# Kernel optimization log

Hardware: AMD Instinct MI355X
Metric: run time of the kernel (lower is better)

## Reference

```python
import jax, jax.numpy as jnp
import numpy as np


def _next_pow2(n: int) -> int:
    return 1 << (int(n) - 1).bit_length()


def setup_inputs() -> dict:
    key = jax.random.key(0)
    k1, k2 = jax.random.split(key)
    B, T, L = 256, 65536, 65536  # batch, seq_len, filter length (L >= T so epoched recurrence == full causal conv)
    x = jax.random.normal(k1, (B, T), dtype=jnp.float32)
    filt = jax.random.normal(k2, (1, L), dtype=jnp.float32) / np.float32(np.sqrt(L))
    return {"x": x, "filt": filt}


def reference(x, filt):
    """EpochedFutureFill.forward == causal FIR convolution of x with filt.

    The torch module's per-token loop (sliced dot-product + FFT-refreshed
    FutureFill cache every K steps) computes exactly
        y[:, t] = sum_{s=0}^{t} filt[0, s] * x[:, t - s]
    for t < T <= L. We express that directly as one FFT convolution,
    mirroring the module's own future_fill (pow-2 rfft/irfft) math.
    """
    B, T = x.shape
    L = filt.shape[-1]
    n_fft = _next_pow2(T + L - 1)
    xf = jnp.fft.rfft(x, n=n_fft)        # (B, n_fft//2+1) complex
    ff = jnp.fft.rfft(filt, n=n_fft)     # (1, n_fft//2+1) complex, broadcasts over batch
    y_full = jnp.fft.irfft(xf * ff, n=n_fft)
    return y_full[:, :T]                 # causal part: (B, T)
```

## Files before the change

### kernel.cpp

```cpp
#include <hip/hip_runtime.h>


#define N_FFT 131072
#define N1    512
#define N2    256
#define T_LEN 65536
#define CB    128
#define PI_F  3.14159265358979323846f
#define R2_F  0.70710678118654752f
#define C16F  0.92387953251128675613f
#define S16F  0.38268343236508977173f

typedef __attribute__((ext_vector_type(2))) __fp16 h2;
typedef __attribute__((ext_vector_type(4))) __fp16 h4;
typedef __attribute__((ext_vector_type(8))) __fp16 h8;

__device__ inline int brev9(int x) { return (int)(__brev((unsigned)x) >> 23); }

__device__ inline float2 cadd(float2 a, float2 b){ return make_float2(a.x+b.x, a.y+b.y); }
__device__ inline float2 csub(float2 a, float2 b){ return make_float2(a.x-b.x, a.y-b.y); }
__device__ inline float2 cmul(float2 a, float2 b){ return make_float2(a.x*b.x-a.y*b.y, a.x*b.y+a.y*b.x); }
__device__ inline float2 cmulc(float2 a, float2 b){ return make_float2(a.x*b.x+a.y*b.y, a.y*b.x-a.x*b.y); }
__device__ inline float2 csq(float2 a){ return make_float2(a.x*a.x-a.y*a.y, 2.f*a.x*a.y); }
__device__ inline float2 conjf(float2 a){ return make_float2(a.x, -a.y); }
__device__ inline float2 expif(float a){ float s,c; __sincosf(a,&s,&c); return make_float2(c,s); }
__device__ inline h2 f2h(float2 v){ return __builtin_amdgcn_cvt_pkrtz(v.x, v.y); }

__device__ inline float2 mul_mi(float2 a){ return make_float2(a.y, -a.x); }
__device__ inline float2 mul_pi(float2 a){ return make_float2(-a.y, a.x); }
__device__ inline float2 mul_w81(float2 a){ return make_float2(R2_F*(a.x+a.y), R2_F*(a.y-a.x)); }
__device__ inline float2 mul_w83(float2 a){ return make_float2(R2_F*(a.y-a.x), -R2_F*(a.x+a.y)); }
__device__ inline float2 mul_w81c(float2 a){ return make_float2(R2_F*(a.x-a.y), R2_F*(a.x+a.y)); }
__device__ inline float2 mul_w83c(float2 a){ return make_float2(-R2_F*(a.x+a.y), R2_F*(a.x-a.y)); }

__device__ inline void dif4(float2&a0, float2&a1, float2&a2, float2&a3, float2 w1, float2 w2){
    float2 s02 = cadd(a0,a2), d02 = csub(a0,a2);
    float2 s13 = cadd(a1,a3), d13 = csub(a1,a3);
    float2 b2 = cmul(w1,d02);
    float2 t  = cmul(w1,d13);
    float2 b3 = make_float2(t.y, -t.x);
    a0 = cadd(s02,s13);
    a1 = cmul(w2, csub(s02,s13));
    a2 = cadd(b2,b3);
    a3 = cmul(w2, csub(b2,b3));
}

__device__ inline void dit4i(float2&a0, float2&a1, float2&a2, float2&a3, float2 w1, float2 w2){
    float2 t1 = cmul(w1,a1), t3 = cmul(w1,a3);
    float2 u0 = cadd(a0,t1), u1 = csub(a0,t1);
    float2 u2 = cadd(a2,t3), u3 = csub(a2,t3);
    float2 s2 = cmul(w2,u2), s3 = cmul(w2,u3);
    a0 = cadd(u0,s2); a2 = csub(u0,s2);
    a1 = make_float2(u1.x - s3.y, u1.y + s3.x);
    a3 = make_float2(u1.x + s3.y, u1.y - s3.x);
}

__device__ constexpr int BR[16] = {0,8,4,12,2,10,6,14,1,9,5,13,3,11,7,15};

__device__ __forceinline__ void fft16_fwd(float2 v[16]){
    {
        float2 s02=cadd(v[0],v[8]),  d02=csub(v[0],v[8]);
        float2 s13=cadd(v[4],v[12]), d13=csub(v[4],v[12]);
        float2 b3 = mul_mi(d13);
        v[0]=cadd(s02,s13); v[4]=csub(s02,s13);
        v[8]=cadd(d02,b3);  v[12]=csub(d02,b3);
    }
    {
        float2 s02=cadd(v[1],v[9]),  d02=csub(v[1],v[9]);
        float2 s13=cadd(v[5],v[13]), d13=csub(v[5],v[13]);
        const float2 w1 = make_float2(C16F,-S16F);
        float2 b2 = cmul(w1,d02), b3 = mul_mi(cmul(w1,d13));
        v[1]=cadd(s02,s13);  v[5]=mul_w81(csub(s02,s13));
        v[9]=cadd(b2,b3);    v[13]=mul_w81(csub(b2,b3));
    }
    {
        float2 s02=cadd(v[2],v[10]), d02=csub(v[2],v[10]);
        float2 s13=cadd(v[6],v[14]), d13=csub(v[6],v[14]);
        float2 b2 = mul_w81(d02), b3 = mul_mi(mul_w81(d13));
        v[2]=cadd(s02,s13);  v[6]=mul_mi(csub(s02,s13));
        v[10]=cadd(b2,b3);   v[14]=mul_mi(csub(b2,b3));
    }
    {
        float2 s02=cadd(v[3],v[11]), d02=csub(v[3],v[11]);
        float2 s13=cadd(v[7],v[15]), d13=csub(v[7],v[15]);
        const float2 w1 = make_float2(S16F,-C16F);
        float2 b2 = cmul(w1,d02), b3 = mul_mi(cmul(w1,d13));
        v[3]=cadd(s02,s13);  v[7]=mul_w83(csub(s02,s13));
        v[11]=cadd(b2,b3);   v[15]=mul_w83(csub(b2,b3));
    }
#pragma unroll
    for (int q=0;q<4;q++){
        float2 a0=v[4*q],a1=v[4*q+1],a2=v[4*q+2],a3=v[4*q+3];
        float2 s02=cadd(a0,a2), d02=csub(a0,a2);
        float2 s13=cadd(a1,a3), d13=csub(a1,a3);
        float2 b3 = mul_mi(d13);
        v[4*q]=cadd(s02,s13);   v[4*q+1]=csub(s02,s13);
        v[4*q+2]=cadd(d02,b3);  v[4*q+3]=csub(d02,b3);
    }
}

__device__ __forceinline__ void fft16_fwd_z8(float2 v[16]){
    {
        float2 a=v[0], b=v[4];
        float2 ib = mul_mi(b);
        v[0]=cadd(a,b); v[4]=csub(a,b);
        v[8]=cadd(a,ib); v[12]=csub(a,ib);
    }
    {
        float2 a=v[1], b=v[5];
        const float2 w1 = make_float2(C16F,-S16F);
        float2 wa = cmul(w1,a), wb = mul_mi(cmul(w1,b));
        v[1]=cadd(a,b);   v[5]=mul_w81(csub(a,b));
        v[9]=cadd(wa,wb); v[13]=mul_w81(csub(wa,wb));
    }
    {
        float2 a=v[2], b=v[6];
        float2 wa = mul_w81(a), wb = mul_mi(mul_w81(b));
        v[2]=cadd(a,b);    v[6]=mul_mi(csub(a,b));
        v[10]=cadd(wa,wb); v[14]=mul_mi(csub(wa,wb));
    }
    {
        float2 a=v[3], b=v[7];
        const float2 w1 = make_float2(S16F,-C16F);
        float2 wa = cmul(w1,a), wb = mul_mi(cmul(w1,b));
        v[3]=cadd(a,b);    v[7]=mul_w83(csub(a,b));
        v[11]=cadd(wa,wb); v[15]=mul_w83(csub(wa,wb));
    }
#pragma unroll
    for (int q=0;q<4;q++){
        float2 a0=v[4*q],a1=v[4*q+1],a2=v[4*q+2],a3=v[4*q+3];
        float2 s02=cadd(a0,a2), d02=csub(a0,a2);
        float2 s13=cadd(a1,a3), d13=csub(a1,a3);
        float2 b3 = mul_mi(d13);
        v[4*q]=cadd(s02,s13);   v[4*q+1]=csub(s02,s13);
        v[4*q+2]=cadd(d02,b3);  v[4*q+3]=csub(d02,b3);
    }
}

__device__ __forceinline__ void fft16_inv(float2 v[16]){
#pragma unroll
    for (int q=0;q<4;q++){
        float2 a0=v[4*q],a1=v[4*q+1],a2=v[4*q+2],a3=v[4*q+3];
        float2 u0=cadd(a0,a1), u1=csub(a0,a1);
        float2 u2=cadd(a2,a3), u3=csub(a2,a3);
        v[4*q]=cadd(u0,u2);   v[4*q+2]=csub(u0,u2);
        v[4*q+1]=make_float2(u1.x-u3.y, u1.y+u3.x);
        v[4*q+3]=make_float2(u1.x+u3.y, u1.y-u3.x);
    }
    {
        float2 t1=v[4], t3=v[12];
        float2 u0=cadd(v[0],t1), u1=csub(v[0],t1);
        float2 u2=cadd(v[8],t3), u3=csub(v[8],t3);
        v[0]=cadd(u0,u2); v[8]=csub(u0,u2);
        v[4]=make_float2(u1.x-u3.y, u1.y+u3.x);
        v[12]=make_float2(u1.x+u3.y, u1.y-u3.x);
    }
    {
        float2 t1=mul_w81c(v[5]), t3=mul_w81c(v[13]);
        float2 u0=cadd(v[1],t1), u1=csub(v[1],t1);
        float2 u2=cadd(v[9],t3), u3=csub(v[9],t3);
        const float2 w2 = make_float2(C16F,S16F);
        float2 s2=cmul(w2,u2), s3=cmul(w2,u3);
        v[1]=cadd(u0,s2); v[9]=csub(u0,s2);
        v[5]=make_float2(u1.x-s3.y, u1.y+s3.x);
        v[13]=make_float2(u1.x+s3.y, u1.y-s3.x);
    }
    {
        float2 t1=mul_pi(v[6]), t3=mul_pi(v[14]);
        float2 u0=cadd(v[2],t1), u1=csub(v[2],t1);
        float2 u2=cadd(v[10],t3), u3=csub(v[10],t3);
        float2 s2=mul_w81c(u2), s3=mul_w81c(u3);
        v[2]=cadd(u0,s2); v[10]=csub(u0,s2);
        v[6]=make_float2(u1.x-s3.y, u1.y+s3.x);
        v[14]=make_float2(u1.x+s3.y, u1.y-s3.x);
    }
    {
        float2 t1=mul_w83c(v[7]), t3=mul_w83c(v[15]);
        float2 u0=cadd(v[3],t1), u1=csub(v[3],t1);
        float2 u2=cadd(v[11],t3), u3=csub(v[11],t3);
        const float2 w2 = make_float2(S16F,C16F);
        float2 s2=cmul(w2,u2), s3=cmul(w2,u3);
        v[3]=cadd(u0,s2); v[11]=csub(u0,s2);
        v[7]=make_float2(u1.x-s3.y, u1.y+s3.x);
        v[15]=make_float2(u1.x+s3.y, u1.y-s3.x);
    }
}

#define XPC 34
#define XPN 546

template<bool HALF>
__global__ __launch_bounds__(256, 4) void fwd_cols(
    const float* __restrict__ re_base, const float* __restrict__ im_base,
    long long row_stride, void* __restrict__ dstv)
{
    __shared__ __align__(16) float2 s[8 * XPN + 32 * 17];
    const int tid = threadIdx.x;
    const int tile = blockIdx.x, row = blockIdx.y;
    const int n2base = tile * 8;
    float2* tab = s + 8 * XPN;

    {
        int q = tid >> 4, c = tid & 15;
        tab[q * 17 + c]        = expif((float)(q * c) * (-2.f * PI_F / 512.f));
        tab[(q + 16) * 17 + c] = expif((float)((q + 16) * c) * (-2.f * PI_F / 512.f));
    }
    __syncthreads();

    const int n2l = tid & 7, q = tid >> 3;
    const float* rp = re_base + (long long)row * row_stride;
    const float* ip = im_base ? (im_base + (long long)row * row_stride) : nullptr;

    float2 v[16];
    if (ip) {
#pragma unroll
        for (int p = 0; p < 8; p++) {
            int g = (32 * p + q) * N2 + n2base + n2l;
            v[p] = make_float2(rp[g], ip[g]);
        }
    } else {
#pragma unroll
        for (int p = 0; p < 8; p++) {
            int g = (32 * p + q) * N2 + n2base + n2l;
            v[p] = make_float2(rp[g], 0.f);
        }
    }
    fft16_fwd_z8(v);

#pragma unroll
    for (int c = 1; c < 16; c++) v[BR[c]] = cmul(v[BR[c]], tab[q * 17 + c]);
#pragma unroll
    for (int c = 0; c < 16; c++) s[n2l * XPN + c * XPC + q] = v[BR[c]];
    __syncthreads();

    const int sI = tid >> 3;
    const int cc = sI & 15, jj = sI >> 4;
    const float4* z4 = (const float4*)(s + n2l * XPN + cc * XPC);
    float2 b[16];
    if (jj == 0) {
#pragma unroll
        for (int k = 0; k < 8; k++) {
            float4 A = z4[k], B = z4[k + 8];
            b[2*k]   = make_float2(A.x + B.x, A.y + B.y);
            b[2*k+1] = make_float2(A.z + B.z, A.w + B.w);
        }
    } else {
        constexpr float CT[16] = {
            1.f, 0.98078528040323044913f, 0.92387953251128675613f, 0.83146961230254523708f,
            0.70710678118654752440f, 0.55557023301960222474f, 0.38268343236508977173f,
            0.19509032201612826785f, 0.f, -0.19509032201612826785f, -0.38268343236508977173f,
            -0.55557023301960222474f, -0.70710678118654752440f, -0.83146961230254523708f,
            -0.92387953251128675613f, -0.98078528040323044913f };
        constexpr float ST[16] = {
            0.f, -0.19509032201612826785f, -0.38268343236508977173f, -0.55557023301960222474f,
            -0.70710678118654752440f, -0.83146961230254523708f, -0.92387953251128675613f,
            -0.98078528040323044913f, -1.f, -0.98078528040323044913f, -0.92387953251128675613f,
            -0.83146961230254523708f, -0.70710678118654752440f, -0.55557023301960222474f,
            -0.38268343236508977173f, -0.19509032201612826785f };
#pragma unroll
        for (int k = 0; k < 8; k++) {
            float4 A = z4[k], B = z4[k + 8];
            float2 d0 = make_float2(A.x - B.x, A.y - B.y);
            float2 d1 = make_float2(A.z - B.z, A.w - B.w);
            b[2*k]   = (k == 0) ? d0 : cmul(d0, make_float2(CT[2*k], ST[2*k]));
            b[2*k+1] = cmul(d1, make_float2(CT[2*k+1], ST[2*k+1]));
        }
    }
    fft16_fwd(b);

    const int n2 = n2base + n2l;
    const float th = -2.f * PI_F / (float)N_FFT;
    float2 w   = expif(th * (float)(n2 * (cc + 16 * jj)));
    float2 stp = expif(th * (float)(32 * n2));
#pragma unroll
    for (int m = 0; m < 16; m++) {
        float2 rv = cmul(b[BR[m]], w);
        int k1 = cc + 32 * m + 16 * jj;
        if (HALF) {
            h2* drow = (h2*)dstv + (size_t)row * N_FFT;
            drow[(size_t)k1 * N2 + n2] = f2h(rv);
        } else {
            float2* drow = (float2*)dstv + (size_t)row * N_FFT;
            drow[(size_t)k1 * N2 + n2] = rv;
        }
        if (m < 15) w = cmul(w, stp);
    }
}

#define RPITCH 18

__global__ __launch_bounds__(128) void fwd_rows_g(float2* __restrict__ G)
{
    __shared__ __align__(16) float2 s[8 * 16 * RPITCH + 16 * RPITCH];
    const int tid = threadIdx.x;
    const int t = tid & 15, rl = tid >> 4;
    const long long row = (long long)blockIdx.x * 8 + rl;
    float2* tab = s + 8 * 16 * RPITCH;

    {
        int b0 = tid >> 4, c0 = tid & 15;
        tab[b0 * RPITCH + c0] = expif((float)(b0 * c0) * (-2.f * PI_F / 256.f));
        int e = tid + 128, b1 = e >> 4, c1 = e & 15;
        tab[b1 * RPITCH + c1] = expif((float)(b1 * c1) * (-2.f * PI_F / 256.f));
    }
    __syncthreads();

    const float2* gp = G + (size_t)row * N2 + t;
    float2 v[16];
#pragma unroll
    for (int a = 0; a < 16; a++) v[a] = gp[16 * a];

    fft16_fwd(v);
#pragma unroll
    for (int p = 1; p < 16; p++) v[p] = cmul(v[p], tab[t * RPITCH + BR[p]]);

    float2* rS = s + rl * (16 * RPITCH);
    float4* rS4 = (float4*)rS;
#pragma unroll
    for (int k = 0; k < 8; k++) {
        float2 e = v[BR[2*k]], o = v[BR[2*k] + 8];
        rS4[(t * RPITCH + 2*k) >> 1] = make_float4(e.x, e.y, o.x, o.y);
    }
    asm volatile("s_waitcnt lgkmcnt(0)" ::: "memory");
#pragma unroll
    for (int b = 0; b < 16; b++) v[b] = rS[b * RPITCH + t];

    fft16_fwd(v);

    float4* o4 = (float4*)(G + (size_t)row * N2 + 16 * t);
#pragma unroll
    for (int m = 0; m < 8; m++)
        o4[m] = make_float4(v[2*m].x, v[2*m].y, v[2*m+1].x, v[2*m+1].y);
}

__global__ __launch_bounds__(256, 4) void mid_rows(
    h2* __restrict__ buf, const float2* __restrict__ Gh)
{
    __shared__ __align__(16) float2 s[16 * 16 * RPITCH + 16 * RPITCH];
    const int tid = threadIdx.x;
    const int t = tid & 15, rl = tid >> 4;
    const long long row = (long long)blockIdx.x * 16 + rl;
    const int k1 = (int)(row & (N1 - 1));
    float2* tab = s + 16 * 16 * RPITCH;

    {
        int b = tid >> 4, c = tid & 15;
        tab[b * RPITCH + c] = expif((float)(b * c) * (-2.f * PI_F / 256.f));
    }
    __syncthreads();

    h2* bp = buf + ((size_t)row * N2 + t);
    float2 v[16];
#pragma unroll
    for (int a = 0; a < 16; a++) {
        h2 h = bp[16 * a];
        v[a] = make_float2((float)h.x, (float)h.y);
    }

    fft16_fwd(v);
#pragma unroll
    for (int p = 1; p < 16; p++) v[p] = cmul(v[p], tab[t * RPITCH + BR[p]]);

    float2* rS = s + rl * (16 * RPITCH);
    float4* rS4 = (float4*)rS;
#pragma unroll
    for (int k = 0; k < 8; k++) {
        float2 e = v[BR[2*k]], o = v[BR[2*k] + 8];
        rS4[(t * RPITCH + 2*k) >> 1] = make_float4(e.x, e.y, o.x, o.y);
    }

    const float4* g4 = (const float4*)(Gh + ((size_t)k1 * N2 + 16 * t));
    float4 g[8];
#pragma unroll
    for (int m = 0; m < 8; m++) g[m] = g4[m];

    asm volatile("s_waitcnt lgkmcnt(0)" ::: "memory");
#pragma unroll
    for (int b = 0; b < 16; b++) v[b] = rS[b * RPITCH + t];

    fft16_fwd(v);

#pragma unroll
    for (int m = 0; m < 8; m++) {
        v[2*m]   = cmul(v[2*m],   make_float2(g[m].x, g[m].y));
        v[2*m+1] = cmul(v[2*m+1], make_float2(g[m].z, g[m].w));
    }

    fft16_inv(v);
#pragma unroll
    for (int b = 1; b < 16; b++) v[b] = cmulc(v[b], tab[b * RPITCH + t]);

#pragma unroll
    for (int m = 0; m < 8; m++)
        rS4[(t * RPITCH + 2*m) >> 1] = make_float4(v[2*m].x, v[2*m].y, v[2*m+1].x, v[2*m+1].y);
    asm volatile("s_waitcnt lgkmcnt(0)" ::: "memory");
#pragma unroll
    for (int c = 0; c < 16; c++) v[BR[c]] = rS[c * RPITCH + t];

    fft16_inv(v);

    {
        const float th = 2.f * PI_F / (float)N_FFT;
        float2 w = expif((float)(k1 * t) * th);
        const float2 stp = expif((float)(16 * k1) * th);
#pragma unroll
        for (int a = 0; a < 16; a++) {
            float2 r = cmul(v[a], w);
            bp[16 * a] = f2h(r);
            if (a < 15) w = cmul(w, stp);
        }
    }
}

__global__ __launch_bounds__(512, 4) void inv_cols(
    const h2* __restrict__ src, float* __restrict__ out)
{
    __shared__ float4 s4[N1 * 16 / 2];
    float2* s = (float2*)s4;
    const int tile = blockIdx.x, row = blockIdx.y, tid = threadIdx.x;
    const int n2base = tile * 16;
    const h2* srow = src + (size_t)row * N_FFT;
    const int cp = tid & 7, r8 = tid >> 3;

#pragma unroll
    for (int i = 0; i < 8; i++) {
        int k1 = r8 + 64 * i;
        h4 v = *((const h4*)(srow + (size_t)k1 * N2 + n2base + 2 * cp));
        int p = brev9(k1);
        s4[p * 8 + cp] = make_float4((float)v.x, (float)v.y, (float)v.z, (float)v.w);
    }
    __syncthreads();

    const int c = tid & 15, r = tid >> 4;

    const float2 w1c = make_float2(0.f, 1.f);
    const float2 w2c = make_float2(R2_F, R2_F);
    const float2 one = make_float2(1.f, 0.f);
#pragma unroll
    for (int o = 0; o < 2; o++) {
        int base = 8 * (r + 32 * o);
        float2 v[8];
#pragma unroll
        for (int m = 0; m < 8; m++) v[m] = s[(base + m) * 16 + c];
#pragma unroll
        for (int m = 0; m < 8; m += 2) {
            float2 a = v[m], b = v[m + 1];
            v[m] = cadd(a, b); v[m + 1] = csub(a, b);
        }
        dit4i(v[0], v[2], v[4], v[6], one, one);
        dit4i(v[1], v[3], v[5], v[7], w1c, w2c);
#pragma unroll
        for (int m = 0; m < 8; m++) s[(base + m) * 16 + c] = v[m];
    }
    __syncthreads();

    {
        float2 w2 = expif((float)(r & 7) * (PI_F / 16.f));
        float2 w1 = csq(w2);
#pragma unroll
        for (int qq = 0; qq < 4; qq++) {
            int g = (r >> 3) + 4 * qq;
            int p0 = g * 32 + (r & 7);
            float2 a0 = s[p0*16+c], a1 = s[(p0+8)*16+c], a2 = s[(p0+16)*16+c], a3 = s[(p0+24)*16+c];
            dit4i(a0, a1, a2, a3, w1, w2);
            s[p0*16+c] = a0; s[(p0+8)*16+c] = a1; s[(p0+16)*16+c] = a2; s[(p0+24)*16+c] = a3;
        }
    }
    __syncthreads();
    {
        float2 w2 = expif((float)r * (PI_F / 64.f));
        float2 w1 = csq(w2);
#pragma unroll
        for (int qq = 0; qq < 4; qq++) {
            int p0 = qq * 128 + r;
            float2 a0 = s[p0*16+c], a1 = s[(p0+32)*16+c], a2 = s[(p0+64)*16+c], a3 = s[(p0+96)*16+c];
            dit4i(a0, a1, a2, a3, w1, w2);
            s[p0*16+c] = a0; s[(p0+32)*16+c] = a1; s[(p0+64)*16+c] = a2; s[(p0+96)*16+c] = a3;
        }
    }
    __syncthreads();
    {
        float2 w2 = expif((float)r * (PI_F / 256.f));
        const float2 stp = make_float2(0.92387953251f, 0.38268343236f);
#pragma unroll
        for (int qq = 0; qq < 4; qq++) {
            int j = r + 32 * qq;
            float2 w1 = csq(w2);
            float2 a0 = s[j*16+c], a1 = s[(j+128)*16+c], a2 = s[(j+256)*16+c], a3 = s[(j+384)*16+c];
            dit4i(a0, a1, a2, a3, w1, w2);
            s[j*16+c] = a0; s[(j+128)*16+c] = a1; s[(j+256)*16+c] = a2; s[(j+384)*16+c] = a3;
            w2 = cmul(w2, stp);
        }
    }
    __syncthreads();

    const float scale = 1.0f / (float)N_FFT;
    float* out0 = out + (size_t)(2 * row) * T_LEN;
    float* out1 = out + (size_t)(2 * row + 1) * T_LEN;
#pragma unroll
    for (int i = 0; i < 4; i++) {
        int p = r8 + 64 * i;
        float4 q = s4[p * 8 + cp];
        int n = p * N2 + n2base + 2 * cp;
        *(float2*)(out0 + n) = make_float2(q.x * scale, q.z * scale);
        *(float2*)(out1 + n) = make_float2(q.y * scale, q.w * scale);
    }
}

extern "C" void kernel_launch(void* const* d_in, const int* in_sizes, int n_in,
                              void* d_out, int out_size, void* d_ws, size_t ws_size,
                              hipStream_t stream) {
    const float* x    = (const float*)d_in[0];
    const float* filt = (const float*)d_in[1];
    float* out = (float*)d_out;

    h2* buf = (h2*)d_ws;
    float2* G = (float2*)((char*)d_ws + (size_t)CB * N_FFT * sizeof(h2));

    fwd_cols<false><<<dim3(32, 1), 256, 0, stream>>>(filt, nullptr, 0LL, (void*)G);
    fwd_rows_g<<<N1 / 8, 128, 0, stream>>>(G);
    fwd_cols<true><<<dim3(32, CB), 256, 0, stream>>>(x, x + T_LEN, (long long)(2 * T_LEN), (void*)buf);
    mid_rows<<<(CB * N1) / 16, 256, 0, stream>>>(buf, G);
    inv_cols<<<dim3(16, CB), 512, 0, stream>>>(buf, out);
}
```

Baseline: 244.1 us.

## Restructure forward column FFT to 16 columns per block with even/odd split

The forward column FFT kernel now processes 16 columns per block, half as many blocks. Each thread loads 16 full samples, where it used to load 8 zero-padded ones, and forms an even/odd pair of 16-point FFTs using constant twiddles. The shared twiddle table and its initial syncthreads are replaced by an incremental twiddle recurrence. The shared-memory exchange is split into two halves separated by lightweight lgkmcnt barriers, and the results feed a second 16-point FFT per half. This cuts block count and shared-memory table setup, but raises register pressure and serialises work into two phases per block.

```diff
diff --git a/kernel.cpp b/kernel.cpp
--- a/kernel.cpp
+++ b/kernel.cpp
@@ -32,6 +32,12 @@
 __device__ inline float2 mul_w83(float2 a){ return make_float2(R2_F*(a.y-a.x), -R2_F*(a.x+a.y)); }
 __device__ inline float2 mul_w81c(float2 a){ return make_float2(R2_F*(a.x-a.y), R2_F*(a.x+a.y)); }
 __device__ inline float2 mul_w83c(float2 a){ return make_float2(-R2_F*(a.x+a.y), R2_F*(a.x-a.y)); }
+
+__device__ __forceinline__ void lgkm_barrier(){
+    asm volatile("s_waitcnt lgkmcnt(0)" ::: "memory");
+    __builtin_amdgcn_s_barrier();
+    __builtin_amdgcn_sched_barrier(0);
+}
 
 __device__ inline void dif4(float2&a0, float2&a1, float2&a2, float2&a3, float2 w1, float2 w2){
     float2 s02 = cadd(a0,a2), d02 = csub(a0,a2);
@@ -99,44 +105,6 @@
     }
 }
 
-__device__ __forceinline__ void fft16_fwd_z8(float2 v[16]){
-    {
-        float2 a=v[0], b=v[4];
-        float2 ib = mul_mi(b);
-        v[0]=cadd(a,b); v[4]=csub(a,b);
-        v[8]=cadd(a,ib); v[12]=csub(a,ib);
-    }
-    {
-        float2 a=v[1], b=v[5];
-        const float2 w1 = make_float2(C16F,-S16F);
-        float2 wa = cmul(w1,a), wb = mul_mi(cmul(w1,b));
-        v[1]=cadd(a,b);   v[5]=mul_w81(csub(a,b));
-        v[9]=cadd(wa,wb); v[13]=mul_w81(csub(wa,wb));
-    }
-    {
-        float2 a=v[2], b=v[6];
-        float2 wa = mul_w81(a), wb = mul_mi(mul_w81(b));
-        v[2]=cadd(a,b);    v[6]=mul_mi(csub(a,b));
-        v[10]=cadd(wa,wb); v[14]=mul_mi(csub(wa,wb));
-    }
-    {
-        float2 a=v[3], b=v[7];
-        const float2 w1 = make_float2(S16F,-C16F);
-        float2 wa = cmul(w1,a), wb = mul_mi(cmul(w1,b));
-        v[3]=cadd(a,b);    v[7]=mul_w83(csub(a,b));
-        v[11]=cadd(wa,wb); v[15]=mul_w83(csub(wa,wb));
-    }
-#pragma unroll
-    for (int q=0;q<4;q++){
-        float2 a0=v[4*q],a1=v[4*q+1],a2=v[4*q+2],a3=v[4*q+3];
-        float2 s02=cadd(a0,a2), d02=csub(a0,a2);
-        float2 s13=cadd(a1,a3), d13=csub(a1,a3);
-        float2 b3 = mul_mi(d13);
-        v[4*q]=cadd(s02,s13);   v[4*q+1]=csub(s02,s13);
-        v[4*q+2]=cadd(d02,b3);  v[4*q+3]=csub(d02,b3);
-    }
-}
-
 __device__ __forceinline__ void fft16_inv(float2 v[16]){
 #pragma unroll
     for (int q=0;q<4;q++){
@@ -186,104 +154,100 @@
     }
 }
 
-#define XPC 34
-#define XPN 546
-
 template<bool HALF>
 __global__ __launch_bounds__(256, 4) void fwd_cols(
     const float* __restrict__ re_base, const float* __restrict__ im_base,
     long long row_stride, void* __restrict__ dstv)
 {
-    __shared__ __align__(16) float2 s[8 * XPN + 32 * 17];
+    __shared__ __align__(16) float2 s[16 * 290];
     const int tid = threadIdx.x;
     const int tile = blockIdx.x, row = blockIdx.y;
-    const int n2base = tile * 8;
-    float2* tab = s + 8 * XPN;
-
-    {
-        int q = tid >> 4, c = tid & 15;
-        tab[q * 17 + c]        = expif((float)(q * c) * (-2.f * PI_F / 512.f));
-        tab[(q + 16) * 17 + c] = expif((float)((q + 16) * c) * (-2.f * PI_F / 512.f));
-    }
-    __syncthreads();
-
-    const int n2l = tid & 7, q = tid >> 3;
+    const int n2base = tile * 16;
+    const int n2l = tid & 15, q = tid >> 4;
+    const int n2 = n2base + n2l;
+
     const float* rp = re_base + (long long)row * row_stride;
     const float* ip = im_base ? (im_base + (long long)row * row_stride) : nullptr;
 
-    float2 v[16];
+    float2 vE[16], vO[16];
     if (ip) {
 #pragma unroll
-        for (int p = 0; p < 8; p++) {
-            int g = (32 * p + q) * N2 + n2base + n2l;
-            v[p] = make_float2(rp[g], ip[g]);
+        for (int p = 0; p < 16; p++) {
+            int g = (16 * p + q) * N2 + n2;
+            vE[p] = make_float2(rp[g], ip[g]);
         }
     } else {
 #pragma unroll
-        for (int p = 0; p < 8; p++) {
-            int g = (32 * p + q) * N2 + n2base + n2l;
-            v[p] = make_float2(rp[g], 0.f);
-        }
-    }
-    fft16_fwd_z8(v);
-
-#pragma unroll
-    for (int c = 1; c < 16; c++) v[BR[c]] = cmul(v[BR[c]], tab[q * 17 + c]);
-#pragma unroll
-    for (int c = 0; c < 16; c++) s[n2l * XPN + c * XPC + q] = v[BR[c]];
-    __syncthreads();
-
-    const int sI = tid >> 3;
-    const int cc = sI & 15, jj = sI >> 4;
-    const float4* z4 = (const float4*)(s + n2l * XPN + cc * XPC);
-    float2 b[16];
-    if (jj == 0) {
-#pragma unroll
-        for (int k = 0; k < 8; k++) {
-            float4 A = z4[k], B = z4[k + 8];
-            b[2*k]   = make_float2(A.x + B.x, A.y + B.y);
-            b[2*k+1] = make_float2(A.z + B.z, A.w + B.w);
-        }
-    } else {
-        constexpr float CT[16] = {
+        for (int p = 0; p < 16; p++) {
+            int g = (16 * p + q) * N2 + n2;
+            vE[p] = make_float2(rp[g], 0.f);
+        }
+    }
+    {
+        constexpr float WC[16] = {
             1.f, 0.98078528040323044913f, 0.92387953251128675613f, 0.83146961230254523708f,
             0.70710678118654752440f, 0.55557023301960222474f, 0.38268343236508977173f,
             0.19509032201612826785f, 0.f, -0.19509032201612826785f, -0.38268343236508977173f,
             -0.55557023301960222474f, -0.70710678118654752440f, -0.83146961230254523708f,
             -0.92387953251128675613f, -0.98078528040323044913f };
-        constexpr float ST[16] = {
+        constexpr float WS[16] = {
             0.f, -0.19509032201612826785f, -0.38268343236508977173f, -0.55557023301960222474f,
             -0.70710678118654752440f, -0.83146961230254523708f, -0.92387953251128675613f,
             -0.98078528040323044913f, -1.f, -0.98078528040323044913f, -0.92387953251128675613f,
             -0.83146961230254523708f, -0.70710678118654752440f, -0.55557023301960222474f,
             -0.38268343236508977173f, -0.19509032201612826785f };
-#pragma unroll
-        for (int k = 0; k < 8; k++) {
-            float4 A = z4[k], B = z4[k + 8];
-            float2 d0 = make_float2(A.x - B.x, A.y - B.y);
-            float2 d1 = make_float2(A.z - B.z, A.w - B.w);
-            b[2*k]   = (k == 0) ? d0 : cmul(d0, make_float2(CT[2*k], ST[2*k]));
-            b[2*k+1] = cmul(d1, make_float2(CT[2*k+1], ST[2*k+1]));
-        }
-    }
-    fft16_fwd(b);
-
-    const int n2 = n2base + n2l;
-    const float th = -2.f * PI_F / (float)N_FFT;
-    float2 w   = expif(th * (float)(n2 * (cc + 16 * jj)));
-    float2 stp = expif(th * (float)(32 * n2));
-#pragma unroll
-    for (int m = 0; m < 16; m++) {
-        float2 rv = cmul(b[BR[m]], w);
-        int k1 = cc + 32 * m + 16 * jj;
-        if (HALF) {
-            h2* drow = (h2*)dstv + (size_t)row * N_FFT;
-            drow[(size_t)k1 * N2 + n2] = f2h(rv);
-        } else {
-            float2* drow = (float2*)dstv + (size_t)row * N_FFT;
-            drow[(size_t)k1 * N2 + n2] = rv;
-        }
-        if (m < 15) w = cmul(w, stp);
+        vO[0] = vE[0];
+#pragma unroll
+        for (int p = 1; p < 16; p++) vO[p] = cmul(vE[p], make_float2(WC[p], WS[p]));
+    }
+    fft16_fwd(vE);
+    fft16_fwd(vO);
+
+    const float2 u = expif((float)q * (-2.f * PI_F / 512.f));
+    float2 w = make_float2(1.f, 0.f);
+    const int exbase = n2l * 290;
+    const float thN = -2.f * PI_F / (float)N_FFT;
+    const float2 stpN = expif(thN * (float)(32 * n2));
+
+#pragma unroll
+    for (int h = 0; h < 2; h++) {
+#pragma unroll
+        for (int t = 0; t < 8; t++) {
+            int tt = t + 8 * h;
+            int rl = 2 * t;
+            s[exbase + rl * 18 + q]       = cmul(vE[BR[tt]], w);  w = cmul(w, u);
+            s[exbase + (rl + 1) * 18 + q] = cmul(vO[BR[tt]], w);  w = cmul(w, u);
+        }
+        lgkm_barrier();
+
+        float2 b[16];
+        {
+            const float4* z4 = (const float4*)(s + exbase + q * 18);
+#pragma unroll
+            for (int j = 0; j < 8; j++) {
+                float4 A = z4[j];
+                b[2*j]   = make_float2(A.x, A.y);
+                b[2*j+1] = make_float2(A.z, A.w);
+            }
+        }
+        fft16_fwd(b);
+
+        const int rpr = 16 * h + q;
+        float2 wb = expif(thN * (float)(n2 * rpr));
+#pragma unroll
+        for (int m = 0; m < 16; m++) {
+            float2 rv = cmul(b[BR[m]], wb);
+            int k1 = rpr + 32 * m;
+            if (HALF) {
+                h2* drow = (h2*)dstv + (size_t)row * N_FFT;
+                drow[(size_t)k1 * N2 + n2] = f2h(rv);
+            } else {
+                float2* drow = (float2*)dstv + (size_t)row * N_FFT;
+                drow[(size_t)k1 * N2 + n2] = rv;
+            }
+            if (m < 15) wb = cmul(wb, stpN);
+        }
+        if (h == 0) lgkm_barrier();
     }
 }
 
@@ -517,9 +481,9 @@
     h2* buf = (h2*)d_ws;
     float2* G = (float2*)((char*)d_ws + (size_t)CB * N_FFT * sizeof(h2));
 
-    fwd_cols<false><<<dim3(32, 1), 256, 0, stream>>>(filt, nullptr, 0LL, (void*)G);
+    fwd_cols<false><<<dim3(16, 1), 256, 0, stream>>>(filt, nullptr, 0LL, (void*)G);
     fwd_rows_g<<<N1 / 8, 128, 0, stream>>>(G);
-    fwd_cols<true><<<dim3(32, CB), 256, 0, stream>>>(x, x + T_LEN, (long long)(2 * T_LEN), (void*)buf);
+    fwd_cols<true><<<dim3(16, CB), 256, 0, stream>>>(x, x + T_LEN, (long long)(2 * T_LEN), (void*)buf);
     mid_rows<<<(CB * N1) / 16, 256, 0, stream>>>(buf, G);
     inv_cols<<<dim3(16, CB), 512, 0, stream>>>(buf, out);
 }
```

After: 224.2 us. 1.09x faster.

## Restructure forward column FFT into 16-column tiles with two-pass LDS exchange

Applied to the files above, without the earlier changes.

The forward column kernel now handles 16 columns per block with 512 threads instead of 8 columns with 256. Shared-memory use is halved by running the 512-point exchange in two halves through a smaller buffer. The stored twiddle table is replaced by an on-the-fly recurrence of complex multiplies, and __syncthreads is replaced by a custom lgkmcnt wait plus s_barrier. The goal is to widen coalesced global loads, reduce LDS footprint to raise occupancy, and cut setup cost. In exchange it adds an extra barrier round, and the twiddle recurrence may lose some accuracy.

```diff
diff --git a/kernel.cpp b/kernel.cpp
--- a/kernel.cpp
+++ b/kernel.cpp
@@ -32,6 +32,12 @@
 __device__ inline float2 mul_w83(float2 a){ return make_float2(R2_F*(a.y-a.x), -R2_F*(a.x+a.y)); }
 __device__ inline float2 mul_w81c(float2 a){ return make_float2(R2_F*(a.x-a.y), R2_F*(a.x+a.y)); }
 __device__ inline float2 mul_w83c(float2 a){ return make_float2(-R2_F*(a.x+a.y), R2_F*(a.x-a.y)); }
+
+__device__ __forceinline__ void lgkm_barrier(){
+    asm volatile("s_waitcnt lgkmcnt(0)" ::: "memory");
+    __builtin_amdgcn_s_barrier();
+    __builtin_amdgcn_sched_barrier(0);
+}
 
 __device__ inline void dif4(float2&a0, float2&a1, float2&a2, float2&a3, float2 w1, float2 w2){
     float2 s02 = cadd(a0,a2), d02 = csub(a0,a2);
@@ -186,28 +192,21 @@
     }
 }
 
-#define XPC 34
-#define XPN 546
+#define FPC 34
+#define FPN 274
 
 template<bool HALF>
-__global__ __launch_bounds__(256, 4) void fwd_cols(
+__global__ __launch_bounds__(512, 8) void fwd_cols(
     const float* __restrict__ re_base, const float* __restrict__ im_base,
     long long row_stride, void* __restrict__ dstv)
 {
-    __shared__ __align__(16) float2 s[8 * XPN + 32 * 17];
+    __shared__ __align__(16) float2 s[16 * FPN];
     const int tid = threadIdx.x;
     const int tile = blockIdx.x, row = blockIdx.y;
-    const int n2base = tile * 8;
-    float2* tab = s + 8 * XPN;
-
-    {
-        int q = tid >> 4, c = tid & 15;
-        tab[q * 17 + c]        = expif((float)(q * c) * (-2.f * PI_F / 512.f));
-        tab[(q + 16) * 17 + c] = expif((float)((q + 16) * c) * (-2.f * PI_F / 512.f));
-    }
-    __syncthreads();
-
-    const int n2l = tid & 7, q = tid >> 3;
+    const int n2base = tile * 16;
+    const int n2l = tid & 15, q = tid >> 4;
+    const int n2 = n2base + n2l;
+
     const float* rp = re_base + (long long)row * row_stride;
     const float* ip = im_base ? (im_base + (long long)row * row_stride) : nullptr;
 
@@ -215,75 +214,94 @@
     if (ip) {
 #pragma unroll
         for (int p = 0; p < 8; p++) {
-            int g = (32 * p + q) * N2 + n2base + n2l;
+            int g = (32 * p + q) * N2 + n2;
             v[p] = make_float2(rp[g], ip[g]);
         }
     } else {
 #pragma unroll
         for (int p = 0; p < 8; p++) {
-            int g = (32 * p + q) * N2 + n2base + n2l;
+            int g = (32 * p + q) * N2 + n2;
             v[p] = make_float2(rp[g], 0.f);
         }
     }
     fft16_fwd_z8(v);
 
-#pragma unroll
-    for (int c = 1; c < 16; c++) v[BR[c]] = cmul(v[BR[c]], tab[q * 17 + c]);
-#pragma unroll
-    for (int c = 0; c < 16; c++) s[n2l * XPN + c * XPC + q] = v[BR[c]];
-    __syncthreads();
-
-    const int sI = tid >> 3;
-    const int cc = sI & 15, jj = sI >> 4;
-    const float4* z4 = (const float4*)(s + n2l * XPN + cc * XPC);
-    float2 b[16];
-    if (jj == 0) {
-#pragma unroll
-        for (int k = 0; k < 8; k++) {
-            float4 A = z4[k], B = z4[k + 8];
-            b[2*k]   = make_float2(A.x + B.x, A.y + B.y);
-            b[2*k+1] = make_float2(A.z + B.z, A.w + B.w);
-        }
-    } else {
-        constexpr float CT[16] = {
-            1.f, 0.98078528040323044913f, 0.92387953251128675613f, 0.83146961230254523708f,
-            0.70710678118654752440f, 0.55557023301960222474f, 0.38268343236508977173f,
-            0.19509032201612826785f, 0.f, -0.19509032201612826785f, -0.38268343236508977173f,
-            -0.55557023301960222474f, -0.70710678118654752440f, -0.83146961230254523708f,
-            -0.92387953251128675613f, -0.98078528040323044913f };
-        constexpr float ST[16] = {
-            0.f, -0.19509032201612826785f, -0.38268343236508977173f, -0.55557023301960222474f,
-            -0.70710678118654752440f, -0.83146961230254523708f, -0.92387953251128675613f,
-            -0.98078528040323044913f, -1.f, -0.98078528040323044913f, -0.92387953251128675613f,
-            -0.83146961230254523708f, -0.70710678118654752440f, -0.55557023301960222474f,
-            -0.38268343236508977173f, -0.19509032201612826785f };
-#pragma unroll
-        for (int k = 0; k < 8; k++) {
-            float4 A = z4[k], B = z4[k + 8];
-            float2 d0 = make_float2(A.x - B.x, A.y - B.y);
-            float2 d1 = make_float2(A.z - B.z, A.w - B.w);
-            b[2*k]   = (k == 0) ? d0 : cmul(d0, make_float2(CT[2*k], ST[2*k]));
-            b[2*k+1] = cmul(d1, make_float2(CT[2*k+1], ST[2*k+1]));
-        }
-    }
-    fft16_fwd(b);
-
-    const int n2 = n2base + n2l;
-    const float th = -2.f * PI_F / (float)N_FFT;
-    float2 w   = expif(th * (float)(n2 * (cc + 16 * jj)));
-    float2 stp = expif(th * (float)(32 * n2));
-#pragma unroll
-    for (int m = 0; m < 16; m++) {
-        float2 rv = cmul(b[BR[m]], w);
-        int k1 = cc + 32 * m + 16 * jj;
-        if (HALF) {
-            h2* drow = (h2*)dstv + (size_t)row * N_FFT;
-            drow[(size_t)k1 * N2 + n2] = f2h(rv);
-        } else {
-            float2* drow = (float2*)dstv + (size_t)row * N_FFT;
-            drow[(size_t)k1 * N2 + n2] = rv;
-        }
-        if (m < 15) w = cmul(w, stp);
+    {
+        const float2 u = expif((float)q * (-2.f * PI_F / 512.f));
+        float2 w = u;
+#pragma unroll
+        for (int c = 1; c < 16; c++) {
+            v[BR[c]] = cmul(v[BR[c]], w);
+            if (c < 15) w = cmul(w, u);
+        }
+    }
+
+    const int cI  = q & 15, jj = q >> 4;
+    const int clR = cI & 7, twin = cI >> 3;
+    const float thN = -2.f * PI_F / (float)N_FFT;
+    const float2 stpN = expif(thN * (float)(32 * n2));
+    const int exb = n2l * FPN;
+
+#pragma unroll
+    for (int h = 0; h < 2; h++) {
+#pragma unroll
+        for (int cl = 0; cl < 8; cl++)
+            s[exb + cl * FPC + q] = v[BR[8 * h + cl]];
+        lgkm_barrier();
+
+        float2 b[16];
+        {
+            const float4* z4 = (const float4*)(s + exb + clR * FPC);
+            if (jj == 0) {
+#pragma unroll
+                for (int k = 0; k < 8; k++) {
+                    float4 A = z4[k], B = z4[k + 8];
+                    b[2*k]   = make_float2(A.x + B.x, A.y + B.y);
+                    b[2*k+1] = make_float2(A.z + B.z, A.w + B.w);
+                }
+            } else {
+                constexpr float CT[16] = {
+                    1.f, 0.98078528040323044913f, 0.92387953251128675613f, 0.83146961230254523708f,
+                    0.70710678118654752440f, 0.55557023301960222474f, 0.38268343236508977173f,
+                    0.19509032201612826785f, 0.f, -0.19509032201612826785f, -0.38268343236508977173f,
+                    -0.55557023301960222474f, -0.70710678118654752440f, -0.83146961230254523708f,
+                    -0.92387953251128675613f, -0.98078528040323044913f };
+                constexpr float ST[16] = {
+                    0.f, -0.19509032201612826785f, -0.38268343236508977173f, -0.55557023301960222474f,
+                    -0.70710678118654752440f, -0.83146961230254523708f, -0.92387953251128675613f,
+                    -0.98078528040323044913f, -1.f, -0.98078528040323044913f, -0.92387953251128675613f,
+                    -0.83146961230254523708f, -0.70710678118654752440f, -0.55557023301960222474f,
+                    -0.38268343236508977173f, -0.19509032201612826785f };
+#pragma unroll
+                for (int k = 0; k < 8; k++) {
+                    float4 A = z4[k], B = z4[k + 8];
+                    float2 d0 = make_float2(A.x - B.x, A.y - B.y);
+                    float2 d1 = make_float2(A.z - B.z, A.w - B.w);
+                    b[2*k]   = (k == 0) ? d0 : cmul(d0, make_float2(CT[2*k], ST[2*k]));
+                    b[2*k+1] = cmul(d1, make_float2(CT[2*k+1], ST[2*k+1]));
+                }
+            }
+        }
+        fft16_fwd(b);
+
+        const int cc = 8 * h + clR;
+        const int k1b = cc + 16 * jj;
+        float2 wb = expif(thN * (float)(n2 * (k1b + 256 * twin)));
+#pragma unroll
+        for (int mm = 0; mm < 8; mm++) {
+            int m = 8 * twin + mm;
+            float2 rv = cmul(b[BR[m]], wb);
+            int k1 = k1b + 32 * m;
+            if (HALF) {
+                h2* drow = (h2*)dstv + (size_t)row * N_FFT;
+                drow[(size_t)k1 * N2 + n2] = f2h(rv);
+            } else {
+                float2* drow = (float2*)dstv + (size_t)row * N_FFT;
+                drow[(size_t)k1 * N2 + n2] = rv;
+            }
+            if (mm < 7) wb = cmul(wb, stpN);
+        }
+        if (h == 0) lgkm_barrier();
     }
 }
 
@@ -517,9 +535,9 @@
     h2* buf = (h2*)d_ws;
     float2* G = (float2*)((char*)d_ws + (size_t)CB * N_FFT * sizeof(h2));
 
-    fwd_cols<false><<<dim3(32, 1), 256, 0, stream>>>(filt, nullptr, 0LL, (void*)G);
+    fwd_cols<false><<<dim3(16, 1), 512, 0, stream>>>(filt, nullptr, 0LL, (void*)G);
     fwd_rows_g<<<N1 / 8, 128, 0, stream>>>(G);
-    fwd_cols<true><<<dim3(32, CB), 256, 0, stream>>>(x, x + T_LEN, (long long)(2 * T_LEN), (void*)buf);
+    fwd_cols<true><<<dim3(16, CB), 512, 0, stream>>>(x, x + T_LEN, (long long)(2 * T_LEN), (void*)buf);
     mid_rows<<<(CB * N1) / 16, 256, 0, stream>>>(buf, G);
     inv_cols<<<dim3(16, CB), 512, 0, stream>>>(buf, out);
 }
```

New measurement: 568.5 us. 133% more time.
